# Performance work log

Measured on AMD Instinct MI355X. Metric: run time of the kernel, lower is better.

Reference implementation:

```python
import jax, jax.numpy as jnp
import numpy as np

B, K, F, E = 32, 1024, 128, 128  # batch, window_size(num_nodes), n_features, embed_dim
OUT2 = 125                       # lin2 output dim (hardcoded in module)
ALPHA = 0.2                      # LeakyReLU negative slope


def setup_inputs() -> dict:
    key = jax.random.key(0)
    ks = jax.random.split(key, 7)
    x = jax.random.normal(ks[0], (B, K, F), dtype=jnp.float32)
    lin_w = jax.random.normal(ks[1], (E, F), dtype=jnp.float32) * 0.05
    lin_b = jax.random.normal(ks[2], (E,), dtype=jnp.float32) * 0.01
    a = jax.random.normal(ks[3], (2 * E, 1), dtype=jnp.float32) * 0.1  # xavier-ish
    bias = jax.random.normal(ks[4], (K, K), dtype=jnp.float32) * 0.02
    lin2_w = jax.random.normal(ks[5], (OUT2, K), dtype=jnp.float32) * 0.03
    lin2_b = jax.random.normal(ks[6], (OUT2,), dtype=jnp.float32) * 0.01
    return {"x": x, "lin_w": lin_w, "lin_b": lin_b, "a": a, "bias": bias,
            "lin2_w": lin2_w, "lin2_b": lin2_b}


def reference(x, lin_w, lin_b, a, bias, lin2_w, lin2_b):
    # Wx = lin(x): [B,K,E]
    Wx = jnp.einsum('bkf,ef->bke', x, lin_w) + lin_b
    # Additive attention scores. Original concatenates (Wx_i, Wx_j) -> [B,K,K,2E]
    # then matmuls with a [2E,1]. Identity: concat @ a == Wx_i@a1 + Wx_j@a2.
    a1 = a[:E, 0]   # [E]
    a2 = a[E:, 0]   # [E]
    s1 = Wx @ a1    # [B,K]  (row/query term, from repeat_interleave)
    s2 = Wx @ a2    # [B,K]  (col/key term, from repeat)
    e = jax.nn.leaky_relu(s1[:, :, None] + s2[:, None, :], negative_slope=ALPHA)
    e = e + bias                              # [B,K,K]
    attention = jax.nn.softmax(e, axis=2)     # softmax over last dim (keys)
    h = jnp.einsum('bij,bjf->bif', attention, x) + x   # [B,K,F], residual
    # permute(0,2,1) -> [B,F,K]; lin2 contracts K -> 125
    h2 = jnp.einsum('bkf,ok->bfo', h, lin2_w) + lin2_b  # [B,F,125]
    h2 = jax.nn.relu(h2)
    return (h2, attention)
```

## Files before the change

kernel.cpp:

```cpp
#include <hip/hip_runtime.h>

#define B_ 32
#define K_ 1024
#define F_ 128
#define E_ 128
#define OUT2_ 125
#define ALPHA_ 0.2f

typedef __bf16 bf16x8_t __attribute__((ext_vector_type(8)));
typedef float  f32x4_t  __attribute__((ext_vector_type(4)));

__global__ __launch_bounds__(256) void k_xts(const float* __restrict__ x,
                                             const float* __restrict__ lin_w,
                                             const float* __restrict__ lin_b,
                                             const float* __restrict__ a,
                                             unsigned short* __restrict__ xt,
                                             float* __restrict__ s1,
                                             float* __restrict__ s2) {
    int kt = blockIdx.x;
    int b  = blockIdx.y;
    int t  = threadIdx.x;
    __shared__ float xs[64 * 132];
    __shared__ float red1[4][64], red2[4][64];
    __shared__ float wsl[260];

    {
        int f = t & 127, sel = t >> 7;
        const float* av = a + sel * 128;
        float acc = 0.f;
#pragma unroll 8
        for (int e = 0; e < E_; ++e) acc += lin_w[e * F_ + f] * av[e];
        wsl[sel * 128 + f] = acc;
        if (t < 2) {
            const float* aw = a + t * 128;
            float c = 0.f;
#pragma unroll 8
            for (int e = 0; e < E_; ++e) c += lin_b[e] * aw[e];
            wsl[256 + t] = c;
        }
    }
    const float* xb = x + ((size_t)b * K_ + kt * 64) * F_;
#pragma unroll
    for (int q = 0; q < 8; ++q) {
        int flat = q * 256 + t;
        int kk = flat >> 5, f4 = flat & 31;
        float4 v = *(const float4*)(xb + (size_t)kk * F_ + f4 * 4);
        xs[kk * 132 + f4 * 4]     = v.x;
        xs[kk * 132 + f4 * 4 + 1] = v.y;
        xs[kk * 132 + f4 * 4 + 2] = v.z;
        xs[kk * 132 + f4 * 4 + 3] = v.w;
    }
    __syncthreads();
    {
        int f = t >> 1, half = t & 1;
        union { __bf16 h[32]; uint4 v[4]; } pack;
#pragma unroll
        for (int i = 0; i < 32; ++i) pack.h[i] = (__bf16)xs[(half * 32 + i) * 132 + f];
        unsigned short* dst = xt + (((size_t)(b * 16 + kt) * 128 + f) * 64 + half * 32);
        uint4* d4 = (uint4*)dst;
#pragma unroll
        for (int i = 0; i < 4; ++i) d4[i] = pack.v[i];
    }
    {
        int r = t & 63, p = t >> 6;
        const float4* xr = (const float4*)&xs[r * 132 + p * 32];
        const float4* w1 = (const float4*)&wsl[p * 32];
        const float4* w2 = (const float4*)&wsl[128 + p * 32];
        float a1 = 0.f, a2 = 0.f;
#pragma unroll
        for (int q = 0; q < 8; ++q) {
            float4 xv = xr[q];
            float4 wa = w1[q], wb = w2[q];
            a1 += xv.x * wa.x + xv.y * wa.y + xv.z * wa.z + xv.w * wa.w;
            a2 += xv.x * wb.x + xv.y * wb.y + xv.z * wb.z + xv.w * wb.w;
        }
        red1[p][r] = a1; red2[p][r] = a2;
    }
    __syncthreads();
    if (t < 64) {
        s1[(size_t)b * K_ + kt * 64 + t] =
            red1[0][t] + red1[1][t] + red1[2][t] + red1[3][t] + wsl[256];
    } else if (t < 128) {
        int r = t - 64;
        s2[(size_t)b * K_ + kt * 64 + r] =
            red2[0][r] + red2[1][r] + red2[2][r] + red2[3][r] + wsl[257];
    }
}

__global__ __launch_bounds__(256) void k_softmax(const float* __restrict__ s1,
                                                 const float* __restrict__ s2,
                                                 const float* __restrict__ bias,
                                                 float* __restrict__ att) {
    int i = blockIdx.x >> 5;
    int b = blockIdx.x & 31;
    int t = threadIdx.x;
    float sv = s1[b * K_ + i];
    float4 s2v = ((const float4*)(s2 + b * K_))[t];
    float4 bv  = ((const float4*)(bias + (size_t)i * K_))[t];
    float e[4];
    {
        float v;
        v = sv + s2v.x; v = v > 0.f ? v : ALPHA_ * v; e[0] = __expf(v + bv.x);
        v = sv + s2v.y; v = v > 0.f ? v : ALPHA_ * v; e[1] = __expf(v + bv.y);
        v = sv + s2v.z; v = v > 0.f ? v : ALPHA_ * v; e[2] = __expf(v + bv.z);
        v = sv + s2v.w; v = v > 0.f ? v : ALPHA_ * v; e[3] = __expf(v + bv.w);
    }
    float sum = e[0] + e[1] + e[2] + e[3];
    for (int m = 32; m; m >>= 1) sum += __shfl_xor(sum, m, 64);
    __shared__ float reds[4];
    int wave = t >> 6, lane = t & 63;
    if (lane == 0) reds[wave] = sum;
    __syncthreads();
    sum = reds[0] + reds[1] + reds[2] + reds[3];
    float r = 1.f / sum;
    float4 o; o.x = e[0] * r; o.y = e[1] * r; o.z = e[2] * r; o.w = e[3] * r;
    ((float4*)(att + ((size_t)b * K_ + i) * K_))[t] = o;
}

__global__ __launch_bounds__(256, 4) void k_attx(const float* __restrict__ att,
                                                 const unsigned short* __restrict__ xt,
                                                 const float* __restrict__ x,
                                                 unsigned short* __restrict__ ht) {
    int b  = blockIdx.y;
    int i0 = blockIdx.x * 32;
    int t  = threadIdx.x;
    int wave = t >> 6, lane = t & 63;
    int quad = lane >> 4, l15 = lane & 15;

    __shared__ unsigned short X_s[2][128 * 64];

    const float* ab  = att + ((size_t)b * K_ + i0) * K_;
    const uint4* xtb = (const uint4*)(xt + (size_t)b * 16 * 128 * 64);

    const float* arow[2];
    arow[0] = ab + (size_t)l15 * K_ + quad * 8;
    arow[1] = arow[0] + 16 * K_;

    f32x4_t acc[2][2];
#pragma unroll
    for (int m = 0; m < 2; ++m)
#pragma unroll
        for (int n = 0; n < 2; ++n) acc[m][n] = (f32x4_t)(0.f);

    bf16x8_t afc[2][2];
    {
        float4 av[2][2][2];
#pragma unroll
        for (int m = 0; m < 2; ++m)
#pragma unroll
            for (int kh = 0; kh < 2; ++kh) {
                av[m][kh][0] = *(const float4*)(arow[m] + kh * 32);
                av[m][kh][1] = *(const float4*)(arow[m] + kh * 32 + 4);
            }
#pragma unroll
        for (int q = 0; q < 4; ++q) {
            int flat = q * 256 + t;
            int row = flat >> 3, g = flat & 7;
            *(uint4*)&X_s[0][row * 64 + 8 * (g ^ (row & 7))] = xtb[flat];
        }
#pragma unroll
        for (int m = 0; m < 2; ++m)
#pragma unroll
            for (int kh = 0; kh < 2; ++kh) {
                union { __bf16 h[8]; bf16x8_t v; } p;
                float4 v0 = av[m][kh][0], v1 = av[m][kh][1];
                p.h[0] = (__bf16)v0.x; p.h[1] = (__bf16)v0.y;
                p.h[2] = (__bf16)v0.z; p.h[3] = (__bf16)v0.w;
                p.h[4] = (__bf16)v1.x; p.h[5] = (__bf16)v1.y;
                p.h[6] = (__bf16)v1.z; p.h[7] = (__bf16)v1.w;
                afc[m][kh] = p.v;
            }
    }
    __syncthreads();

    int cur = 0;
#pragma unroll
    for (int kt = 0; kt < 16; ++kt) {
        uint4 xn[4];
        float4 av[2][2][2];
        if (kt < 15) {
            const uint4* src = xtb + (size_t)(kt + 1) * 1024;
#pragma unroll
            for (int q = 0; q < 4; ++q) xn[q] = src[q * 256 + t];
            int ko = (kt + 1) * 64;
#pragma unroll
            for (int m = 0; m < 2; ++m)
#pragma unroll
                for (int kh = 0; kh < 2; ++kh) {
                    av[m][kh][0] = *(const float4*)(arow[m] + ko + kh * 32);
                    av[m][kh][1] = *(const float4*)(arow[m] + ko + kh * 32 + 4);
                }
        }
#pragma unroll
        for (int kh = 0; kh < 2; ++kh) {
            bf16x8_t bff[2];
#pragma unroll
            for (int n = 0; n < 2; ++n) {
                int row = wave * 32 + n * 16 + l15;
                bff[n] = *(const bf16x8_t*)&X_s[cur][row * 64 + 8 * (((kh << 2) | quad) ^ (row & 7))];
            }
#pragma unroll
            for (int m = 0; m < 2; ++m)
#pragma unroll
                for (int n = 0; n < 2; ++n)
                    acc[m][n] = __builtin_amdgcn_mfma_f32_16x16x32_bf16(afc[m][kh], bff[n], acc[m][n], 0, 0, 0);
        }
        if (kt < 15) {
#pragma unroll
            for (int m = 0; m < 2; ++m)
#pragma unroll
                for (int kh = 0; kh < 2; ++kh) {
                    union { __bf16 h[8]; bf16x8_t v; } p;
                    float4 v0 = av[m][kh][0], v1 = av[m][kh][1];
                    p.h[0] = (__bf16)v0.x; p.h[1] = (__bf16)v0.y;
                    p.h[2] = (__bf16)v0.z; p.h[3] = (__bf16)v0.w;
                    p.h[4] = (__bf16)v1.x; p.h[5] = (__bf16)v1.y;
                    p.h[6] = (__bf16)v1.z; p.h[7] = (__bf16)v1.w;
                    afc[m][kh] = p.v;
                }
#pragma unroll
            for (int q = 0; q < 4; ++q) {
                int flat = q * 256 + t;
                int row = flat >> 3, g = flat & 7;
                *(uint4*)&X_s[cur ^ 1][row * 64 + 8 * (g ^ (row & 7))] = xn[q];
            }
        }
        __syncthreads();
        cur ^= 1;
    }
#pragma unroll
    for (int m = 0; m < 2; ++m) {
#pragma unroll
        for (int n = 0; n < 2; ++n) {
            int f = wave * 32 + n * 16 + l15;
            int ib = i0 + m * 16 + quad * 4;
            union { __bf16 h[4]; ushort4 v; } p;
#pragma unroll
            for (int r = 0; r < 4; ++r) {
                int i = ib + r;
                p.h[r] = (__bf16)(acc[m][n][r] + x[((size_t)b * K_ + i) * F_ + f]);
            }
            *(ushort4*)&ht[((size_t)b * F_ + f) * K_ + ib] = p.v;
        }
    }
}

__global__ __launch_bounds__(256) void k_out2m(const unsigned short* __restrict__ ht,
                                               const float* __restrict__ w2,
                                               float* __restrict__ part) {
    int b  = blockIdx.y;
    int f0 = blockIdx.x * 64;
    int ks = blockIdx.z;
    int t  = threadIdx.x;
    int wave = t >> 6, lane = t & 63;
    int quad = lane >> 4, l15 = lane & 15;

    __shared__ unsigned short W_s[128 * 72];
    __shared__ unsigned short H_s[64 * 72];

    f32x4_t acc[8];
#pragma unroll
    for (int m = 0; m < 8; ++m) acc[m] = (f32x4_t)(0.f);

    int wo = t >> 1, wq = t & 1;
    int hf = t >> 2, hq = t & 3;

    int kt0 = ks * 4;
    for (int kt = kt0; kt < kt0 + 4; ++kt) {
        int k0 = kt * 64;
        __syncthreads();
        {
            union { __bf16 h[32]; uint4 v[4]; } p;
            if (wo < OUT2_) {
                const float* src = w2 + (size_t)wo * K_ + k0 + wq * 32;
#pragma unroll
                for (int q = 0; q < 8; ++q) {
                    float4 v = *(const float4*)(src + q * 4);
                    p.h[q * 4]     = (__bf16)v.x;
                    p.h[q * 4 + 1] = (__bf16)v.y;
                    p.h[q * 4 + 2] = (__bf16)v.z;
                    p.h[q * 4 + 3] = (__bf16)v.w;
                }
            } else {
#pragma unroll
                for (int q = 0; q < 4; ++q) p.v[q] = make_uint4(0, 0, 0, 0);
            }
            uint4* d = (uint4*)&W_s[wo * 72 + wq * 32];
#pragma unroll
            for (int q = 0; q < 4; ++q) d[q] = p.v[q];
        }
        {
            const uint4* src = (const uint4*)(ht + ((size_t)b * F_ + f0 + hf) * K_ + k0) + hq * 2;
            uint4* d = (uint4*)&H_s[hf * 72 + hq * 16];
            d[0] = src[0]; d[1] = src[1];
        }
        __syncthreads();
#pragma unroll
        for (int kh = 0; kh < 2; ++kh) {
            bf16x8_t bf = *(const bf16x8_t*)&H_s[(wave * 16 + l15) * 72 + kh * 32 + quad * 8];
#pragma unroll
            for (int m = 0; m < 8; ++m) {
                bf16x8_t af = *(const bf16x8_t*)&W_s[(m * 16 + l15) * 72 + kh * 32 + quad * 8];
                acc[m] = __builtin_amdgcn_mfma_f32_16x16x32_bf16(af, bf, acc[m], 0, 0, 0);
            }
        }
    }
    int f = f0 + wave * 16 + l15;
    float* prow = part + ((size_t)(ks * 32 + b) * 128 + f) * 128;
#pragma unroll
    for (int m = 0; m < 8; ++m)
        *(f32x4_t*)&prow[m * 16 + quad * 4] = acc[m];
}

__global__ __launch_bounds__(256) void k_out2e(const float* __restrict__ part,
                                               const float* __restrict__ b2,
                                               float* __restrict__ out) {
    int idx = blockIdx.x * 256 + threadIdx.x;
    if (idx >= B_ * F_ * OUT2_) return;
    int o  = idx % OUT2_;
    int bf = idx / OUT2_;
    float v = b2[o];
#pragma unroll
    for (int s = 0; s < 4; ++s) v += part[((size_t)s * 4096 + bf) * 128 + o];
    out[idx] = v > 0.f ? v : 0.f;
}

extern "C" void kernel_launch(void* const* d_in, const int* in_sizes, int n_in,
                              void* d_out, int out_size, void* d_ws, size_t ws_size,
                              hipStream_t stream) {
    const float* x      = (const float*)d_in[0];
    const float* lin_w  = (const float*)d_in[1];
    const float* lin_b  = (const float*)d_in[2];
    const float* a      = (const float*)d_in[3];
    const float* bias   = (const float*)d_in[4];
    const float* lin2_w = (const float*)d_in[5];
    const float* lin2_b = (const float*)d_in[6];

    float* out = (float*)d_out;
    float* h2  = out;
    float* att = out + (size_t)B_ * F_ * OUT2_;

    float* ws = (float*)d_ws;
    float* s1 = ws + 512;
    float* s2 = ws + 512 + B_ * K_;
    unsigned short* ht = (unsigned short*)(ws + 512 + 2 * B_ * K_);
    unsigned short* xt = ht + (size_t)B_ * K_ * F_;
    float* part = (float*)xt;

    k_xts<<<dim3(16, B_), 256, 0, stream>>>(x, lin_w, lin_b, a, xt, s1, s2);
    k_softmax<<<B_ * K_, 256, 0, stream>>>(s1, s2, bias, att);
    k_attx<<<dim3(K_ / 32, B_), 256, 0, stream>>>(att, xt, x, ht);
    k_out2m<<<dim3(2, B_, 4), 256, 0, stream>>>(ht, lin2_w, part);
    k_out2e<<<(B_ * F_ * OUT2_ + 255) / 256, 256, 0, stream>>>(part, lin2_b, h2);
}
```

Baseline: 280.1 us.

## Fuse softmax into attention-times-x kernel with block index swizzle

Removes the separate softmax kernel: each attx block now computes the softmax for its 32 rows (two passes over s2 and bias, recomputing exp), writes the attention output, then reads those rows back for the MFMA stage. This saves one kernel launch and lets the attention rows be reread while likely still in cache instead of after a separate pass. Block indices are swizzled so neighbouring blocks are spread across batches. In exchange each thread computes exp twice per element, and the global write-then-read of att inside the same block relies on the __syncthreads for visibility.

```diff
diff --git a/kernel.cpp b/kernel.cpp
--- a/kernel.cpp
+++ b/kernel.cpp
@@ -87,48 +87,56 @@
     }
 }
 
-__global__ __launch_bounds__(256) void k_softmax(const float* __restrict__ s1,
+__global__ __launch_bounds__(256, 4) void k_attx(const float* __restrict__ s1,
                                                  const float* __restrict__ s2,
                                                  const float* __restrict__ bias,
-                                                 float* __restrict__ att) {
-    int i = blockIdx.x >> 5;
-    int b = blockIdx.x & 31;
-    int t = threadIdx.x;
-    float sv = s1[b * K_ + i];
-    float4 s2v = ((const float4*)(s2 + b * K_))[t];
-    float4 bv  = ((const float4*)(bias + (size_t)i * K_))[t];
-    float e[4];
-    {
-        float v;
-        v = sv + s2v.x; v = v > 0.f ? v : ALPHA_ * v; e[0] = __expf(v + bv.x);
-        v = sv + s2v.y; v = v > 0.f ? v : ALPHA_ * v; e[1] = __expf(v + bv.y);
-        v = sv + s2v.z; v = v > 0.f ? v : ALPHA_ * v; e[2] = __expf(v + bv.z);
-        v = sv + s2v.w; v = v > 0.f ? v : ALPHA_ * v; e[3] = __expf(v + bv.w);
-    }
-    float sum = e[0] + e[1] + e[2] + e[3];
-    for (int m = 32; m; m >>= 1) sum += __shfl_xor(sum, m, 64);
-    __shared__ float reds[4];
-    int wave = t >> 6, lane = t & 63;
-    if (lane == 0) reds[wave] = sum;
-    __syncthreads();
-    sum = reds[0] + reds[1] + reds[2] + reds[3];
-    float r = 1.f / sum;
-    float4 o; o.x = e[0] * r; o.y = e[1] * r; o.z = e[2] * r; o.w = e[3] * r;
-    ((float4*)(att + ((size_t)b * K_ + i) * K_))[t] = o;
-}
-
-__global__ __launch_bounds__(256, 4) void k_attx(const float* __restrict__ att,
                                                  const unsigned short* __restrict__ xt,
                                                  const float* __restrict__ x,
+                                                 float* __restrict__ att,
                                                  unsigned short* __restrict__ ht) {
-    int b  = blockIdx.y;
-    int i0 = blockIdx.x * 32;
+    int flat = blockIdx.y * gridDim.x + blockIdx.x;
+    int swz  = (flat & 7) * 128 + (flat >> 3);
+    int b  = swz >> 5;
+    int i0 = (swz & 31) * 32;
     int t  = threadIdx.x;
     int wave = t >> 6, lane = t & 63;
     int quad = lane >> 4, l15 = lane & 15;
 
     __shared__ unsigned short X_s[2][128 * 64];
 
+    {
+        int ai = t >> 3, aq = t & 7;
+        float sv = s1[b * K_ + i0 + ai];
+        const float4* s2p = (const float4*)(s2 + (size_t)b * K_ + aq * 128);
+        const float4* bp  = (const float4*)(bias + (size_t)(i0 + ai) * K_ + aq * 128);
+        float sum = 0.f;
+#pragma unroll 8
+        for (int c = 0; c < 32; ++c) {
+            float4 s2v = s2p[c], bv = bp[c];
+            float v;
+            v = sv + s2v.x; v = v > 0.f ? v : ALPHA_ * v; sum += __expf(v + bv.x);
+            v = sv + s2v.y; v = v > 0.f ? v : ALPHA_ * v; sum += __expf(v + bv.y);
+            v = sv + s2v.z; v = v > 0.f ? v : ALPHA_ * v; sum += __expf(v + bv.z);
+            v = sv + s2v.w; v = v > 0.f ? v : ALPHA_ * v; sum += __expf(v + bv.w);
+        }
+        sum += __shfl_xor(sum, 1, 64);
+        sum += __shfl_xor(sum, 2, 64);
+        sum += __shfl_xor(sum, 4, 64);
+        float rv = 1.f / sum;
+        float4* ap = (float4*)(att + ((size_t)(b * K_ + i0 + ai)) * K_ + aq * 128);
+#pragma unroll 8
+        for (int c = 0; c < 32; ++c) {
+            float4 s2v = s2p[c], bv = bp[c];
+            float4 o; float v;
+            v = sv + s2v.x; v = v > 0.f ? v : ALPHA_ * v; o.x = __expf(v + bv.x) * rv;
+            v = sv + s2v.y; v = v > 0.f ? v : ALPHA_ * v; o.y = __expf(v + bv.y) * rv;
+            v = sv + s2v.z; v = v > 0.f ? v : ALPHA_ * v; o.z = __expf(v + bv.z) * rv;
+            v = sv + s2v.w; v = v > 0.f ? v : ALPHA_ * v; o.w = __expf(v + bv.w) * rv;
+            ap[c] = o;
+        }
+    }
+    __syncthreads();
+
     const float* ab  = att + ((size_t)b * K_ + i0) * K_;
     const uint4* xtb = (const uint4*)(xt + (size_t)b * 16 * 128 * 64);
 
@@ -154,9 +162,9 @@
             }
 #pragma unroll
         for (int q = 0; q < 4; ++q) {
-            int flat = q * 256 + t;
-            int row = flat >> 3, g = flat & 7;
-            *(uint4*)&X_s[0][row * 64 + 8 * (g ^ (row & 7))] = xtb[flat];
+            int flat2 = q * 256 + t;
+            int row = flat2 >> 3, g = flat2 & 7;
+            *(uint4*)&X_s[0][row * 64 + 8 * (g ^ (row & 7))] = xtb[flat2];
         }
 #pragma unroll
         for (int m = 0; m < 2; ++m)
@@ -220,8 +228,8 @@
                 }
 #pragma unroll
             for (int q = 0; q < 4; ++q) {
-                int flat = q * 256 + t;
-                int row = flat >> 3, g = flat & 7;
+                int flat2 = q * 256 + t;
+                int row = flat2 >> 3, g = flat2 & 7;
                 *(uint4*)&X_s[cur ^ 1][row * 64 + 8 * (g ^ (row & 7))] = xn[q];
             }
         }
@@ -348,8 +356,7 @@
     float* part = (float*)xt;
 
     k_xts<<<dim3(16, B_), 256, 0, stream>>>(x, lin_w, lin_b, a, xt, s1, s2);
-    k_softmax<<<B_ * K_, 256, 0, stream>>>(s1, s2, bias, att);
-    k_attx<<<dim3(K_ / 32, B_), 256, 0, stream>>>(att, xt, x, ht);
+    k_attx<<<dim3(K_ / 32, B_), 256, 0, stream>>>(s1, s2, bias, xt, x, att, ht);
     k_out2m<<<dim3(2, B_, 4), 256, 0, stream>>>(ht, lin2_w, part);
     k_out2e<<<(B_ * F_ * OUT2_ + 255) / 256, 256, 0, stream>>>(part, lin2_b, h2);
 }
```

Result: slower. 323.9 us (+15.6%).
